# Performance work log

Measured on AMD Instinct MI355X. Metric: run time of the kernel, lower is better.

Reference implementation:

```python
import jax, jax.numpy as jnp
import numpy as np

EMBED = 1024
HEADS = 16
HEAD_DIM = EMBED // HEADS


def setup_inputs() -> dict:
    key = jax.random.key(0)
    ks = jax.random.split(key, 7)
    N, S = 2, 2048
    k = jax.random.normal(ks[0], (N, S, EMBED), dtype=jnp.float32)
    q = jax.random.normal(ks[1], (N, S, EMBED), dtype=jnp.float32)
    v = jax.random.normal(ks[2], (N, S, EMBED), dtype=jnp.float32)
    sc = 1.0 / np.sqrt(HEAD_DIM)
    # nn.Linear weights, applied as x @ W.T
    Wk = jax.random.normal(ks[3], (HEAD_DIM, HEAD_DIM), dtype=jnp.float32) * sc
    Wq = jax.random.normal(ks[4], (HEAD_DIM, HEAD_DIM), dtype=jnp.float32) * sc
    Wv = jax.random.normal(ks[5], (HEAD_DIM, HEAD_DIM), dtype=jnp.float32) * sc
    Wo = jax.random.normal(ks[6], (EMBED, EMBED), dtype=jnp.float32) / np.sqrt(EMBED)
    return {"k": k, "q": q, "v": v, "Wk": Wk, "Wq": Wq, "Wv": Wv, "Wo": Wo}


def reference(k, q, v, Wk, Wq, Wv, Wo):
    N, S, _ = q.shape
    # reshape to [N, S, H, D]; per-head projection weights shared across heads
    kh = jnp.einsum('nshd,ed->nshe', k.reshape(N, S, HEADS, HEAD_DIM), Wk)
    qh = jnp.einsum('nshd,ed->nshe', q.reshape(N, S, HEADS, HEAD_DIM), Wq)
    vh = jnp.einsum('nshd,ed->nshe', v.reshape(N, S, HEADS, HEAD_DIM), Wv)
    # energy: [N, H, q_len, k_len]
    energy = jnp.einsum('nqhd,nkhd->nhqk', qh, kh)
    attn = jax.nn.softmax(energy / jnp.sqrt(jnp.float32(HEAD_DIM)), axis=-1)
    out = jnp.einsum('nhqk,nkhd->nqhd', attn, vh).reshape(N, S, EMBED)
    return out @ Wo.T
```

## Files before the change

### kernel.cpp

```cpp
#include <hip/hip_runtime.h>

#define SQ   2048
#define HEADS 16
#define HD   64
#define EMB  1024

typedef __attribute__((ext_vector_type(2))) __fp16 h2;
typedef __attribute__((ext_vector_type(4))) __fp16 h4;
typedef __attribute__((ext_vector_type(8))) __fp16 h8;
typedef __attribute__((ext_vector_type(4))) float f4;
typedef unsigned short USH;
typedef unsigned int   UI;

__device__ __forceinline__ UI pkh(float a, float b) {
    h2 v = __builtin_amdgcn_cvt_pkrtz(a, b);
    return __builtin_bit_cast(UI, v);
}

__device__ __forceinline__ void glds16(const void* g, void* l) {
    __builtin_amdgcn_global_load_lds(
        (const __attribute__((address_space(1))) unsigned int*)g,
        (__attribute__((address_space(3))) unsigned int*)l, 16, 0, 0);
}

__global__ __launch_bounds__(256) void proj_fused(
    const float* __restrict__ q_in, const float* __restrict__ k_in,
    const float* __restrict__ v_in, const float* __restrict__ Wq,
    const float* __restrict__ Wk,   const float* __restrict__ Wv,
    const float* __restrict__ Wo,
    USH* __restrict__ Qh, USH* __restrict__ Kh, USH* __restrict__ Vt,
    USH* __restrict__ Wob)
{
    int t = threadIdx.x;
    if (blockIdx.y == 3) {
        int i = blockIdx.x * 256 + t;
        for (int j = 0; j < 4; ++j) {
            float4 v = ((const float4*)Wo)[i + j * 65536];
            uint2 pk; pk.x = pkh(v.x, v.y); pk.y = pkh(v.z, v.w);
            *(uint2*)(Wob + ((size_t)i + (size_t)j * 65536) * 4) = pk;
        }
        return;
    }
    const float* X = (blockIdx.y == 0) ? q_in : (blockIdx.y == 1) ? k_in : v_in;
    const float* W = (blockIdx.y == 0) ? Wq   : (blockIdx.y == 1) ? Wk   : Wv;
    float scale    = (blockIdx.y == 0) ? 0.18033688011112043f : 1.0f;

    __shared__ __align__(16) USH Xl[256][72];
    __shared__ __align__(16) USH Wl[64][72];

    const float4* Xg = (const float4*)(X + (size_t)blockIdx.x * 16384);
    for (int j = 0; j < 16; ++j) {
        int f = t + j * 256;
        float4 v = Xg[f];
        int row = f >> 4; int col = (f & 15) << 2;
        uint2 pk; pk.x = pkh(v.x, v.y); pk.y = pkh(v.z, v.w);
        *(uint2*)&Xl[row][col] = pk;
    }
    const float4* Wg = (const float4*)W;
    for (int j = 0; j < 4; ++j) {
        int f = t + j * 256;
        float4 v = Wg[f];
        int row = f >> 4; int col = (f & 15) << 2;
        uint2 pk; pk.x = pkh(v.x, v.y); pk.y = pkh(v.z, v.w);
        *(uint2*)&Wl[row][col] = pk;
    }
    __syncthreads();

    int wv = t >> 6, lane = t & 63, l4 = lane & 15, quad = lane >> 4;

    h8 wf[4][2], xf[4][2];
    for (int et = 0; et < 4; ++et)
        for (int ks = 0; ks < 2; ++ks)
            wf[et][ks] = *(const h8*)&Wl[et * 16 + l4][ks * 32 + quad * 8];
    for (int rt = 0; rt < 4; ++rt)
        for (int ks = 0; ks < 2; ++ks)
            xf[rt][ks] = *(const h8*)&Xl[wv * 64 + rt * 16 + l4][ks * 32 + quad * 8];

    f4 acc[4][4];
    for (int et = 0; et < 4; ++et)
        for (int rt = 0; rt < 4; ++rt) acc[et][rt] = (f4)(0.0f);
    for (int et = 0; et < 4; ++et)
        for (int rt = 0; rt < 4; ++rt)
            for (int ks = 0; ks < 2; ++ks)
                acc[et][rt] = __builtin_amdgcn_mfma_f32_16x16x32_f16(
                    wf[et][ks], xf[rt][ks], acc[et][rt], 0, 0, 0);

    if (blockIdx.y == 2) {
        int ns0 = blockIdx.x * 16 + wv * 4;
        int n = ns0 >> 11, s = ns0 & 2047;
        int sswz = s ^ ((quad & 2) << 1);
        for (int et = 0; et < 4; ++et)
            for (int j = 0; j < 4; ++j) {
                int e = et * 16 + quad * 4 + j;
                uint2 pk;
                pk.x = pkh(acc[et][0][j], acc[et][1][j]);
                pk.y = pkh(acc[et][2][j], acc[et][3][j]);
                *(uint2*)(Vt + (((size_t)(n * HEADS + l4) * HD + e) * SQ + sswz)) = pk;
            }
    } else {
        USH* Out = (blockIdx.y == 0) ? Qh : Kh;
        for (int rt = 0; rt < 4; ++rt) {
            int ns = blockIdx.x * 16 + wv * 4 + rt;
            int n = ns >> 11, s = ns & 2047;
            USH* ob = Out + (((size_t)(n * HEADS) + l4) * SQ + s) * HD;
            for (int et = 0; et < 4; ++et) {
                uint2 pk;
                pk.x = pkh(acc[et][rt][0] * scale, acc[et][rt][1] * scale);
                pk.y = pkh(acc[et][rt][2] * scale, acc[et][rt][3] * scale);
                *(uint2*)(ob + et * 16 + quad * 4) = pk;
            }
        }
    }
}

__device__ __forceinline__ void stage_kv(const USH* __restrict__ Kg,
                                         const USH* __restrict__ Vg,
                                         int kt, USH* Kd, USH* Vd,
                                         int w, int lane)
{
#pragma unroll
    for (int j = 0; j < 2; ++j) {
        int s = (w * 2 + j) * 64 + lane;
        int r = s >> 3, c = (s & 7) ^ (r & 7);
        glds16(Kg + kt * 4096 + r * 64 + c * 8, Kd + s * 8);
    }
#pragma unroll
    for (int j = 0; j < 2; ++j) {
        int s = (w * 2 + j) * 64 + lane;
        int r = s >> 3, c = (s & 7) ^ (r & 7);
        glds16(Vg + r * SQ + kt * 64 + c * 8, Vd + s * 8);
    }
}

__global__ __launch_bounds__(256, 4) void attn_kernel(
    const USH* __restrict__ Qh, const USH* __restrict__ Kh,
    const USH* __restrict__ Vt, USH* __restrict__ Oh)
{
    __shared__ union {
        struct { USH K[2][4096]; USH V[2][4096]; } s;
        struct { float Osum[64][68]; float Lsum[64]; } r;
    } lds;

    int t = threadIdx.x, w = t >> 6, lane = t & 63;
    int l4 = lane & 15, quad = lane >> 4;
    int b = blockIdx.x;
    int nh = b & 31;
    int q0 = (b >> 5) * 64;
    const USH* Qg = Qh + ((size_t)nh * SQ + q0) * HD;
    const USH* Kg = Kh + (size_t)nh * SQ * HD;
    const USH* Vg = Vt + (size_t)nh * HD * SQ;

    h8 bq[4][2];
#pragma unroll
    for (int qt = 0; qt < 4; ++qt)
#pragma unroll
        for (int ks = 0; ks < 2; ++ks)
            bq[qt][ks] = *(const h8*)(Qg + (size_t)(qt * 16 + l4) * HD + ks * 32 + quad * 8);

    f4 o[4][4];
#pragma unroll
    for (int dt = 0; dt < 4; ++dt)
#pragma unroll
        for (int qt = 0; qt < 4; ++qt) o[dt][qt] = (f4)(0.0f);
    float lsum[4] = {0.f, 0.f, 0.f, 0.f};

    int key = w * 16 + l4;
    int kslot0 = key * 8 + (quad ^ (key & 7));
    int kslot1 = key * 8 + ((4 + quad) ^ (key & 7));
    int dchunk = w * 2 + (quad >> 1);
    int vbyte  = (((quad ^ (l4 >> 3)) & 1)) * 4;

    stage_kv(Kg, Vg, 0, lds.s.K[0], lds.s.V[0], w, lane);

    for (int kt = 0; kt < SQ / 64; ++kt) {
        int cur = kt & 1;
        __syncthreads();
        if (kt + 1 < SQ / 64)
            stage_kv(Kg, Vg, kt + 1, lds.s.K[cur ^ 1], lds.s.V[cur ^ 1], w, lane);

        h8 ak0 = *(const h8*)(lds.s.K[cur] + kslot0 * 8);
        h8 ak1 = *(const h8*)(lds.s.K[cur] + kslot1 * 8);

        h4 p[4];
#pragma unroll
        for (int qt = 0; qt < 4; ++qt) {
            f4 s0 = __builtin_amdgcn_mfma_f32_16x16x32_f16(ak0, bq[qt][0], (f4)(0.0f), 0, 0, 0);
            f4 sc = __builtin_amdgcn_mfma_f32_16x16x32_f16(ak1, bq[qt][1], s0, 0, 0, 0);
            float p0 = __builtin_amdgcn_exp2f(sc[0]);
            float p1 = __builtin_amdgcn_exp2f(sc[1]);
            float p2 = __builtin_amdgcn_exp2f(sc[2]);
            float p3 = __builtin_amdgcn_exp2f(sc[3]);
            lsum[qt] += (p0 + p1) + (p2 + p3);
            uint2 u; u.x = pkh(p0, p1); u.y = pkh(p2, p3);
            p[qt] = __builtin_bit_cast(h4, u);
        }

        __builtin_amdgcn_sched_barrier(0);

        h4 av[4];
#pragma unroll
        for (int dt = 0; dt < 4; ++dt) {
            int d = dt * 16 + l4;
            int vs = d * 8 + (dchunk ^ (d & 7));
            av[dt] = *(const h4*)(lds.s.V[cur] + vs * 8 + vbyte);
        }

#pragma unroll
        for (int dt = 0; dt < 4; ++dt)
#pragma unroll
            for (int qt = 0; qt < 4; ++qt)
                o[dt][qt] = __builtin_amdgcn_mfma_f32_16x16x16f16(
                    av[dt], p[qt], o[dt][qt], 0, 0, 0);
    }

#pragma unroll
    for (int qt = 0; qt < 4; ++qt) {
        lsum[qt] += __shfl_xor(lsum[qt], 16, 64);
        lsum[qt] += __shfl_xor(lsum[qt], 32, 64);
    }

    __syncthreads();
    for (int ph = 0; ph < 4; ++ph) {
        if (w == ph) {
            for (int dt = 0; dt < 4; ++dt)
                for (int qt = 0; qt < 4; ++qt) {
                    float* dst = &lds.r.Osum[qt * 16 + l4][dt * 16 + quad * 4];
                    f4 val = o[dt][qt];
                    if (ph) val += *(const f4*)dst;
                    *(f4*)dst = val;
                }
            if (quad == 0)
                for (int qt = 0; qt < 4; ++qt) {
                    int qi = qt * 16 + l4;
                    lds.r.Lsum[qi] = ph ? (lds.r.Lsum[qi] + lsum[qt]) : lsum[qt];
                }
        }
        __syncthreads();
    }

    int n = nh >> 4, h = nh & 15;
    int q = t >> 2, d0 = (t & 3) * 16;
    float inv = 1.0f / lds.r.Lsum[q];
    float vv[16];
#pragma unroll
    for (int i = 0; i < 4; ++i) {
        f4 x = *(const f4*)&lds.r.Osum[q][d0 + i * 4];
        vv[i * 4 + 0] = x[0] * inv; vv[i * 4 + 1] = x[1] * inv;
        vv[i * 4 + 2] = x[2] * inv; vv[i * 4 + 3] = x[3] * inv;
    }
    uint4 ou0, ou1;
    ou0.x = pkh(vv[0], vv[1]);   ou0.y = pkh(vv[2], vv[3]);
    ou0.z = pkh(vv[4], vv[5]);   ou0.w = pkh(vv[6], vv[7]);
    ou1.x = pkh(vv[8], vv[9]);   ou1.y = pkh(vv[10], vv[11]);
    ou1.z = pkh(vv[12], vv[13]); ou1.w = pkh(vv[14], vv[15]);
    USH* ob = Oh + ((size_t)(n * SQ + q0 + q)) * EMB + h * HD + d0;
    *(uint4*)ob = ou0;
    *(uint4*)(ob + 8) = ou1;
}

__global__ __launch_bounds__(256, 4) void gemm_bt(const USH* __restrict__ A,
                                                  const USH* __restrict__ B,
                                                  float* __restrict__ C)
{
    __shared__ __align__(16) USH Al[2][4096];
    __shared__ __align__(16) USH Bl[2][4096];
    int t = threadIdx.x, w = t >> 6, lane = t & 63;
    int l4 = lane & 15, quad = lane >> 4;
    int b = blockIdx.x;
    int m0 = (b & 63) * 64;
    int n0 = (b >> 6) * 64;
    int wm = (w >> 1) * 32, wn = (w & 1) * 32;

    f4 acc[2][2];
    for (int mt = 0; mt < 2; ++mt)
        for (int nt = 0; nt < 2; ++nt) acc[mt][nt] = (f4)(0.0f);

    int aslot[2][2], bslot[2][2];
#pragma unroll
    for (int mt = 0; mt < 2; ++mt)
#pragma unroll
        for (int ks = 0; ks < 2; ++ks) {
            int m = wm + mt * 16 + l4;
            aslot[mt][ks] = m * 8 + ((ks * 4 + quad) ^ (m & 7));
            int nn = wn + mt * 16 + l4;
            bslot[mt][ks] = nn * 8 + ((ks * 4 + quad) ^ (nn & 7));
        }

#pragma unroll
    for (int j = 0; j < 2; ++j) {
        int s = (w * 2 + j) * 64 + lane;
        int r = s >> 3, c = (s & 7) ^ (r & 7);
        glds16(A + (size_t)(m0 + r) * 1024 + c * 8, Al[0] + s * 8);
        glds16(B + (size_t)(n0 + r) * 1024 + c * 8, Bl[0] + s * 8);
    }

    for (int ki = 0; ki < 16; ++ki) {
        int cur = ki & 1;
        __syncthreads();
        if (ki + 1 < 16) {
            int k0 = (ki + 1) * 64;
#pragma unroll
            for (int j = 0; j < 2; ++j) {
                int s = (w * 2 + j) * 64 + lane;
                int r = s >> 3, c = (s & 7) ^ (r & 7);
                glds16(A + (size_t)(m0 + r) * 1024 + k0 + c * 8, Al[cur ^ 1] + s * 8);
                glds16(B + (size_t)(n0 + r) * 1024 + k0 + c * 8, Bl[cur ^ 1] + s * 8);
            }
        }

        h8 a[2][2], bf[2][2];
#pragma unroll
        for (int mt = 0; mt < 2; ++mt)
#pragma unroll
            for (int ks = 0; ks < 2; ++ks) {
                a[mt][ks]  = *(const h8*)(Al[cur] + aslot[mt][ks] * 8);
                bf[mt][ks] = *(const h8*)(Bl[cur] + bslot[mt][ks] * 8);
            }
#pragma unroll
        for (int mt = 0; mt < 2; ++mt)
#pragma unroll
            for (int nt = 0; nt < 2; ++nt)
#pragma unroll
                for (int ks = 0; ks < 2; ++ks)
                    acc[mt][nt] = __builtin_amdgcn_mfma_f32_16x16x32_f16(
                        a[mt][ks], bf[nt][ks], acc[mt][nt], 0, 0, 0);
    }

    for (int mt = 0; mt < 2; ++mt)
        for (int nt = 0; nt < 2; ++nt)
            for (int r = 0; r < 4; ++r)
                C[(size_t)(m0 + wm + mt * 16 + quad * 4 + r) * 1024 +
                  (n0 + wn + nt * 16 + l4)] = acc[mt][nt][r];
}

extern "C" void kernel_launch(void* const* d_in, const int* in_sizes, int n_in,
                              void* d_out, int out_size, void* d_ws, size_t ws_size,
                              hipStream_t stream) {
    const float* k_in = (const float*)d_in[0];
    const float* q_in = (const float*)d_in[1];
    const float* v_in = (const float*)d_in[2];
    const float* Wk   = (const float*)d_in[3];
    const float* Wq   = (const float*)d_in[4];
    const float* Wv   = (const float*)d_in[5];
    const float* Wo   = (const float*)d_in[6];
    float* out = (float*)d_out;

    char* ws = (char*)d_ws;
    USH* Qh  = (USH*)(ws);
    USH* Kh  = (USH*)(ws + 8388608);
    USH* Vt  = (USH*)(ws + 16777216);
    USH* Oh  = (USH*)(ws + 25165824);
    USH* Wob = (USH*)(ws + 33554432);

    proj_fused<<<dim3(256, 4), dim3(256), 0, stream>>>(
        q_in, k_in, v_in, Wq, Wk, Wv, Wo, Qh, Kh, Vt, Wob);
    attn_kernel<<<dim3(1024), dim3(256), 0, stream>>>(Qh, Kh, Vt, Oh);
    gemm_bt<<<dim3(1024), dim3(256), 0, stream>>>(Oh, Wob, out);
}
```

Before: 185.7 us.

## Split attention waves 2x2 over query and key halves

Work is now split across the four waves as a 2x2 grid: two query groups of 32 rows times two key halves of 32 keys per tile. Before, each wave handled all 64 queries for 16 keys. Per wave, the K fragment loads double while the Q fragments, output accumulators and per-tile V fragment reuse are halved, which lowers register pressure. The final cross-wave reduction drops from four phases to two, cutting the number of LDS accumulate passes and barriers. The trade-off is more K LDS reads per wave and a different MFMA accumulation order into each output tile.

```diff
diff --git a/kernel.cpp b/kernel.cpp
--- a/kernel.cpp
+++ b/kernel.cpp
@@ -143,6 +143,7 @@
 
     int t = threadIdx.x, w = t >> 6, lane = t & 63;
     int l4 = lane & 15, quad = lane >> 4;
+    int qg = w >> 1, ws = w & 1;
     int b = blockIdx.x;
     int nh = b & 31;
     int q0 = (b >> 5) * 64;
@@ -150,25 +151,39 @@
     const USH* Kg = Kh + (size_t)nh * SQ * HD;
     const USH* Vg = Vt + (size_t)nh * HD * SQ;
 
-    h8 bq[4][2];
-#pragma unroll
-    for (int qt = 0; qt < 4; ++qt)
+    h8 bq[2][2];
+#pragma unroll
+    for (int qt = 0; qt < 2; ++qt)
 #pragma unroll
         for (int ks = 0; ks < 2; ++ks)
-            bq[qt][ks] = *(const h8*)(Qg + (size_t)(qt * 16 + l4) * HD + ks * 32 + quad * 8);
-
-    f4 o[4][4];
+            bq[qt][ks] = *(const h8*)(Qg + (size_t)(qg * 32 + qt * 16 + l4) * HD +
+                                      ks * 32 + quad * 8);
+
+    f4 o[4][2];
 #pragma unroll
     for (int dt = 0; dt < 4; ++dt)
 #pragma unroll
-        for (int qt = 0; qt < 4; ++qt) o[dt][qt] = (f4)(0.0f);
-    float lsum[4] = {0.f, 0.f, 0.f, 0.f};
-
-    int key = w * 16 + l4;
-    int kslot0 = key * 8 + (quad ^ (key & 7));
-    int kslot1 = key * 8 + ((4 + quad) ^ (key & 7));
-    int dchunk = w * 2 + (quad >> 1);
-    int vbyte  = (((quad ^ (l4 >> 3)) & 1)) * 4;
+        for (int qt = 0; qt < 2; ++qt) o[dt][qt] = (f4)(0.0f);
+    float lsum[2] = {0.f, 0.f};
+
+    int kslot[2][2];
+#pragma unroll
+    for (int ksub = 0; ksub < 2; ++ksub)
+#pragma unroll
+        for (int ks = 0; ks < 2; ++ks) {
+            int key = ws * 32 + ksub * 16 + l4;
+            kslot[ksub][ks] = key * 8 + ((ks * 4 + quad) ^ (key & 7));
+        }
+    int vslot[4][2];
+#pragma unroll
+    for (int dt = 0; dt < 4; ++dt)
+#pragma unroll
+        for (int ksub = 0; ksub < 2; ++ksub) {
+            int d = dt * 16 + l4;
+            int lc = ws * 4 + ksub * 2 + (quad >> 1);
+            vslot[dt][ksub] = d * 8 + (lc ^ (d & 7));
+        }
+    int vbyte = ((quad ^ (l4 >> 3)) & 1) * 4;
 
     stage_kv(Kg, Vg, 0, lds.s.K[0], lds.s.V[0], w, lane);
 
@@ -178,60 +193,69 @@
         if (kt + 1 < SQ / 64)
             stage_kv(Kg, Vg, kt + 1, lds.s.K[cur ^ 1], lds.s.V[cur ^ 1], w, lane);
 
-        h8 ak0 = *(const h8*)(lds.s.K[cur] + kslot0 * 8);
-        h8 ak1 = *(const h8*)(lds.s.K[cur] + kslot1 * 8);
-
-        h4 p[4];
-#pragma unroll
-        for (int qt = 0; qt < 4; ++qt) {
-            f4 s0 = __builtin_amdgcn_mfma_f32_16x16x32_f16(ak0, bq[qt][0], (f4)(0.0f), 0, 0, 0);
-            f4 sc = __builtin_amdgcn_mfma_f32_16x16x32_f16(ak1, bq[qt][1], s0, 0, 0, 0);
-            float p0 = __builtin_amdgcn_exp2f(sc[0]);
-            float p1 = __builtin_amdgcn_exp2f(sc[1]);
-            float p2 = __builtin_amdgcn_exp2f(sc[2]);
-            float p3 = __builtin_amdgcn_exp2f(sc[3]);
-            lsum[qt] += (p0 + p1) + (p2 + p3);
-            uint2 u; u.x = pkh(p0, p1); u.y = pkh(p2, p3);
-            p[qt] = __builtin_bit_cast(h4, u);
-        }
+        h8 ak[2][2];
+#pragma unroll
+        for (int ksub = 0; ksub < 2; ++ksub)
+#pragma unroll
+            for (int ks = 0; ks < 2; ++ks)
+                ak[ksub][ks] = *(const h8*)(lds.s.K[cur] + kslot[ksub][ks] * 8);
+
+        h4 p[2][2];
+#pragma unroll
+        for (int ksub = 0; ksub < 2; ++ksub)
+#pragma unroll
+            for (int qt = 0; qt < 2; ++qt) {
+                f4 s0 = __builtin_amdgcn_mfma_f32_16x16x32_f16(
+                    ak[ksub][0], bq[qt][0], (f4)(0.0f), 0, 0, 0);
+                f4 sc = __builtin_amdgcn_mfma_f32_16x16x32_f16(
+                    ak[ksub][1], bq[qt][1], s0, 0, 0, 0);
+                float p0 = __builtin_amdgcn_exp2f(sc[0]);
+                float p1 = __builtin_amdgcn_exp2f(sc[1]);
+                float p2 = __builtin_amdgcn_exp2f(sc[2]);
+                float p3 = __builtin_amdgcn_exp2f(sc[3]);
+                lsum[qt] += (p0 + p1) + (p2 + p3);
+                uint2 u; u.x = pkh(p0, p1); u.y = pkh(p2, p3);
+                p[ksub][qt] = __builtin_bit_cast(h4, u);
+            }
 
         __builtin_amdgcn_sched_barrier(0);
 
-        h4 av[4];
-#pragma unroll
-        for (int dt = 0; dt < 4; ++dt) {
-            int d = dt * 16 + l4;
-            int vs = d * 8 + (dchunk ^ (d & 7));
-            av[dt] = *(const h4*)(lds.s.V[cur] + vs * 8 + vbyte);
-        }
-
+        h4 av[4][2];
 #pragma unroll
         for (int dt = 0; dt < 4; ++dt)
 #pragma unroll
-            for (int qt = 0; qt < 4; ++qt)
-                o[dt][qt] = __builtin_amdgcn_mfma_f32_16x16x16f16(
-                    av[dt], p[qt], o[dt][qt], 0, 0, 0);
-    }
-
-#pragma unroll
-    for (int qt = 0; qt < 4; ++qt) {
+            for (int ksub = 0; ksub < 2; ++ksub)
+                av[dt][ksub] = *(const h4*)(lds.s.V[cur] + vslot[dt][ksub] * 8 + vbyte);
+
+#pragma unroll
+        for (int dt = 0; dt < 4; ++dt)
+#pragma unroll
+            for (int qt = 0; qt < 2; ++qt)
+#pragma unroll
+                for (int ksub = 0; ksub < 2; ++ksub)
+                    o[dt][qt] = __builtin_amdgcn_mfma_f32_16x16x16f16(
+                        av[dt][ksub], p[ksub][qt], o[dt][qt], 0, 0, 0);
+    }
+
+#pragma unroll
+    for (int qt = 0; qt < 2; ++qt) {
         lsum[qt] += __shfl_xor(lsum[qt], 16, 64);
         lsum[qt] += __shfl_xor(lsum[qt], 32, 64);
     }
 
     __syncthreads();
-    for (int ph = 0; ph < 4; ++ph) {
-        if (w == ph) {
+    for (int ph = 0; ph < 2; ++ph) {
+        if (ws == ph) {
             for (int dt = 0; dt < 4; ++dt)
-                for (int qt = 0; qt < 4; ++qt) {
-                    float* dst = &lds.r.Osum[qt * 16 + l4][dt * 16 + quad * 4];
+                for (int qt = 0; qt < 2; ++qt) {
+                    float* dst = &lds.r.Osum[qg * 32 + qt * 16 + l4][dt * 16 + quad * 4];
                     f4 val = o[dt][qt];
                     if (ph) val += *(const f4*)dst;
                     *(f4*)dst = val;
                 }
             if (quad == 0)
-                for (int qt = 0; qt < 4; ++qt) {
-                    int qi = qt * 16 + l4;
+                for (int qt = 0; qt < 2; ++qt) {
+                    int qi = qg * 32 + qt * 16 + l4;
                     lds.r.Lsum[qi] = ph ? (lds.r.Lsum[qi] + lsum[qt]) : lsum[qt];
                 }
         }
```

Measured after the change: 188.3 us. No clear change (+1.4%).
